# Kernel tuning notes

Hardware: AMD Instinct MI355X
Metric: run time of the kernel (lower is better)

The kernel has to match this reference:

```python
import jax, jax.numpy as jnp
import numpy as np

S, T, B = 120, 10, 128          # sentence len, word len, batch
E, HW, HS = 80, 75, 700         # embedding, word-GRU hidden, sentence-GRU hidden
V = 30000                       # vocab size


def gru_scan(x, Wih, Whh, bih, bhh):
    """Single-direction GRU (PyTorch gate math). x: [T, N, in] -> (ys [T,N,H], h_T [N,H])."""
    H = Whh.shape[-1]
    xw = jnp.einsum('tni,gi->tng', x, Wih) + bih  # precompute input gates [T,N,3H]

    def step(h, xw_t):
        gh = h @ Whh.T + bhh
        r = jax.nn.sigmoid(xw_t[..., :H] + gh[..., :H])
        z = jax.nn.sigmoid(xw_t[..., H:2 * H] + gh[..., H:2 * H])
        n = jnp.tanh(xw_t[..., 2 * H:] + r * gh[..., 2 * H:])
        h_new = (1.0 - z) * n + z * h
        return h_new, h_new

    h0 = jnp.zeros((x.shape[1], H), x.dtype)
    hT, ys = jax.lax.scan(step, h0, xw)
    return ys, hT


def bigru_layer(x, Wih, Whh, bih, bhh):
    """Bidirectional GRU layer; params have leading dir axis [2,...]."""
    yf, hf = gru_scan(x, Wih[0], Whh[0], bih[0], bhh[0])
    yb, hb = gru_scan(x[::-1], Wih[1], Whh[1], bih[1], bhh[1])
    y = jnp.concatenate([yf, yb[::-1]], axis=-1)
    return y, hf, hb


def setup_inputs() -> dict:
    key = jax.random.key(0)
    ks = iter(jax.random.split(key, 40))

    def p(shape):
        return jax.random.normal(next(ks), shape, jnp.float32) * 0.05

    inp = {'x': jax.random.randint(next(ks), (S, T, B), 0, V)}
    inp['emb'] = p((V, E))
    # word encoder: 2-layer bi-GRU, layer0 in=E, layer1 in=2*HW
    inp['we_Wih0'] = p((2, 3 * HW, E)); inp['we_Whh0'] = p((2, 3 * HW, HW))
    inp['we_bih0'] = p((2, 3 * HW)); inp['we_bhh0'] = p((2, 3 * HW))
    inp['we_Wih1'] = p((2, 3 * HW, 2 * HW)); inp['we_Whh1'] = p((2, 3 * HW, HW))
    inp['we_bih1'] = p((2, 3 * HW)); inp['we_bhh1'] = p((2, 3 * HW))
    # sentence encoder: 2-layer bi-GRU, layer0 in=4*HW=300, layer1 in=2*HS
    inp['se_Wih0'] = p((2, 3 * HS, 4 * HW)); inp['se_Whh0'] = p((2, 3 * HS, HS))
    inp['se_bih0'] = p((2, 3 * HS)); inp['se_bhh0'] = p((2, 3 * HS))
    inp['se_Wih1'] = p((2, 3 * HS, 2 * HS)); inp['se_Whh1'] = p((2, 3 * HS, HS))
    inp['se_bih1'] = p((2, 3 * HS)); inp['se_bhh1'] = p((2, 3 * HS))
    return inp


def reference(x, emb,
              we_Wih0, we_Whh0, we_bih0, we_bhh0,
              we_Wih1, we_Whh1, we_bih1, we_bhh1,
              se_Wih0, se_Whh0, se_bih0, se_bhh0,
              se_Wih1, se_Whh1, se_bih1, se_bhh1):
    # Fold the python loop over 120 sentence positions into the batch:
    # x [S,T,B] -> [T, S*B]
    xt = jnp.transpose(x, (1, 0, 2)).reshape(T, S * B)
    xe = emb[xt]  # [T, S*B, E]
    y0, hf0, hb0 = bigru_layer(xe, we_Wih0, we_Whh0, we_bih0, we_bhh0)
    _, hf1, hb1 = bigru_layer(y0, we_Wih1, we_Whh1, we_bih1, we_bhh1)
    # torch h stacking: [l0_fwd, l0_bwd, l1_fwd, l1_bwd] concat on feature dim
    words = jnp.concatenate([hf0, hb0, hf1, hb1], axis=-1)  # [S*B, 4*HW]
    words = words.reshape(S, B, 4 * HW)
    y0s, sf0, sb0 = bigru_layer(words, se_Wih0, se_Whh0, se_bih0, se_bhh0)
    _, sf1, sb1 = bigru_layer(y0s, se_Wih1, se_Whh1, se_bih1, se_bhh1)
    h = jnp.concatenate([sf0, sb0, sf1, sb1], axis=-1)[None]  # [1, B, 4*HS]
    return h
```

## Files before the change

### kernel.cpp

```cpp
#include <hip/hip_runtime.h>
#include <hip/hip_bf16.h>

typedef __hip_bfloat16 bf16;
typedef __attribute__((ext_vector_type(8))) short bf16x8;
typedef __attribute__((ext_vector_type(4))) short bf16x4;
typedef __attribute__((ext_vector_type(4))) float f32x4;

__device__ __forceinline__ void stC(float* p, float v) { *p = v; }
__device__ __forceinline__ void stC(bf16* p, float v)  { *p = __float2bfloat16(v); }

__device__ __forceinline__ short f2s(float f) {
    bf16 b = __float2bfloat16(f);
    return __builtin_bit_cast(short, b);
}

__device__ __forceinline__ float sigm(float x) {
    x = fminf(fmaxf(x, -40.f), 40.f);
    return 1.f / (1.f + expf(-x));
}
__device__ __forceinline__ float tanh_s(float x) {
    x = fminf(fmaxf(x, -20.f), 20.f);
    float e = expf(2.f * x);
    return 1.f - 2.f / (e + 1.f);
}

__device__ __forceinline__ bf16x8 ld8(const bf16* p) {
    return *reinterpret_cast<const bf16x8*>(p);
}
__device__ __forceinline__ bf16x8 ld8(const float* p) {
    const float4 f0 = *reinterpret_cast<const float4*>(p);
    const float4 f1 = *reinterpret_cast<const float4*>(p + 4);
    bf16x8 v;
    v[0] = f2s(f0.x); v[1] = f2s(f0.y); v[2] = f2s(f0.z); v[3] = f2s(f0.w);
    v[4] = f2s(f1.x); v[5] = f2s(f1.y); v[6] = f2s(f1.z); v[7] = f2s(f1.w);
    return v;
}
__device__ __forceinline__ bf16x8 ld8_8B(const bf16* p) {
    bf16x4 lo = *reinterpret_cast<const bf16x4*>(p);
    bf16x4 hi = *reinterpret_cast<const bf16x4*>(p + 4);
    bf16x8 v;
    v[0] = lo[0]; v[1] = lo[1]; v[2] = lo[2]; v[3] = lo[3];
    v[4] = hi[0]; v[5] = hi[1]; v[6] = hi[2]; v[7] = hi[3];
    return v;
}

__global__ void f2b(const float* __restrict__ src, bf16* __restrict__ dst, long n) {
    long i = (long)blockIdx.x * 256 + threadIdx.x;
    if (i < n) dst[i] = __float2bfloat16(src[i]);
}
__global__ void f2bpad(const float* __restrict__ src, bf16* __restrict__ dst,
                       int rows, int Ks, int Kd) {
    long i = (long)blockIdx.x * 256 + threadIdx.x;
    if (i >= (long)rows * Kd) return;
    int c = i % Kd; long r = i / Kd;
    dst[i] = __float2bfloat16(c < Ks ? src[r * Ks + c] : 0.f);
}
__global__ void f2bremap(const float* __restrict__ src, bf16* __restrict__ dst, int rows) {
    long i = (long)blockIdx.x * 256 + threadIdx.x;
    if (i >= (long)rows * 160) return;
    int c = i % 160; long r = i / 160;
    float v = 0.f;
    if (c < 75) v = src[r * 150 + c];
    else if (c >= 80 && c < 155) v = src[r * 150 + c - 5];
    dst[i] = __float2bfloat16(v);
}

#define MBM 128
#define MBN 64
#define MLD 40

__global__ __launch_bounds__(256) void gemm_mfma(
    const float* __restrict__ A, long sAd,
    const float* __restrict__ W, long sWd,
    bf16* __restrict__ C, long sCd,
    int M, int Nc, int K)
{
    __shared__ bf16 As[MBM * MLD];
    __shared__ bf16 Ws[MBN * MLD];
    const int d = blockIdx.z;
    A += (long)d * sAd; W += (long)d * sWd; C += (long)d * sCd;
    const int m0 = blockIdx.y * MBM;
    const int n0 = blockIdx.x * MBN;
    const int tid = threadIdx.x;
    const int w = tid >> 6, l = tid & 63;
    const int lr = l & 15, lq = l >> 4;

    f32x4 acc[2][4] = {};
    for (int k0 = 0; k0 < K; k0 += 32) {
#pragma unroll
        for (int i = 0; i < 2; ++i) {
            int u = tid + i * 256;
            int r = u >> 2, kk = (u & 3) * 8;
            bf16x8 v = {};
            if (m0 + r < M && k0 + kk < K)
                v = ld8(A + (long)(m0 + r) * K + k0 + kk);
            *reinterpret_cast<bf16x8*>(&As[r * MLD + kk]) = v;
        }
        {
            int r = tid >> 2, kk = (tid & 3) * 8;
            bf16x8 v = {};
            if (n0 + r < Nc && k0 + kk < K)
                v = ld8(W + (long)(n0 + r) * K + k0 + kk);
            *reinterpret_cast<bf16x8*>(&Ws[r * MLD + kk]) = v;
        }
        __syncthreads();
        bf16x8 af[2], bw[4];
        af[0] = *reinterpret_cast<const bf16x8*>(&As[(w * 32 + lr) * MLD + lq * 8]);
        af[1] = *reinterpret_cast<const bf16x8*>(&As[(w * 32 + 16 + lr) * MLD + lq * 8]);
#pragma unroll
        for (int ni = 0; ni < 4; ++ni)
            bw[ni] = *reinterpret_cast<const bf16x8*>(&Ws[(ni * 16 + lr) * MLD + lq * 8]);
#pragma unroll
        for (int mi = 0; mi < 2; ++mi)
#pragma unroll
            for (int ni = 0; ni < 4; ++ni)
                acc[mi][ni] = __builtin_amdgcn_mfma_f32_16x16x32_bf16(
                    af[mi], bw[ni], acc[mi][ni], 0, 0, 0);
        __syncthreads();
    }
#pragma unroll
    for (int mi = 0; mi < 2; ++mi)
#pragma unroll
        for (int reg = 0; reg < 4; ++reg) {
            int m = m0 + w * 32 + mi * 16 + lq * 4 + reg;
            if (m >= M) continue;
#pragma unroll
            for (int ni = 0; ni < 4; ++ni) {
                int n = n0 + ni * 16 + lr;
                if (n < Nc) stC(&C[(long)m * Nc + n], acc[mi][ni][reg]);
            }
        }
}

__global__ __launch_bounds__(256) void gemm_bt(
    const bf16* __restrict__ A, long sAd,
    const bf16* __restrict__ W, long sWd,
    bf16* __restrict__ C, long sCd,
    int M, int Nc, int KP)
{
    __shared__ bf16 As[128 * 64];
    __shared__ bf16 Ws[128 * 64];
    const int d = blockIdx.z;
    A += (long)d * sAd; W += (long)d * sWd; C += (long)d * sCd;
    const int nx = (Nc + 127) >> 7, ny = M >> 7;
    int id = blockIdx.x;
    int band = id / (8 * ny);
    int rr = id - band * 8 * ny;
    int bwd = nx - band * 8; if (bwd > 8) bwd = 8;
    const int bx = band * 8 + rr % bwd;
    const int by = rr / bwd;
    const int m0 = by << 7;
    const int n0 = bx << 7;
    const int tid = threadIdx.x;
    const int w = tid >> 6, l = tid & 63;
    const int lr = l & 15, lq = l >> 4;

    const int sr = tid >> 3;
    const int sg = tid & 7;
    const bf16x8 z8 = {};
    bf16x8 ra[4], rb[4];
    auto stage = [&](int k0) {
        const bool kin = (k0 + sg * 8) < KP;
#pragma unroll
        for (int i = 0; i < 4; ++i)
            ra[i] = kin ? ld8(A + (long)(m0 + sr + i * 32) * KP + k0 + sg * 8) : z8;
#pragma unroll
        for (int i = 0; i < 4; ++i)
            rb[i] = kin ? ld8(W + (long)(n0 + sr + i * 32) * KP + k0 + sg * 8) : z8;
    };

    f32x4 acc[2][8] = {};
    stage(0);
    for (int k0 = 0; k0 < KP; k0 += 64) {
#pragma unroll
        for (int i = 0; i < 4; ++i) {
            const int r = sr + i * 32;
            const int g = sg ^ (r & 7);
            *reinterpret_cast<bf16x8*>(&As[r * 64 + g * 8]) = ra[i];
            *reinterpret_cast<bf16x8*>(&Ws[r * 64 + g * 8]) = rb[i];
        }
        __syncthreads();
        if (k0 + 64 < KP) stage(k0 + 64);
#pragma unroll
        for (int ks = 0; ks < 2; ++ks) {
            const int gb = ks * 4 + lq;
            bf16x8 af[2], bw8[8];
#pragma unroll
            for (int mi = 0; mi < 2; ++mi) {
                const int r = w * 32 + mi * 16 + lr;
                af[mi] = *reinterpret_cast<const bf16x8*>(
                    &As[r * 64 + (gb ^ (r & 7)) * 8]);
            }
#pragma unroll
            for (int ni = 0; ni < 8; ++ni) {
                const int r = ni * 16 + lr;
                bw8[ni] = *reinterpret_cast<const bf16x8*>(
                    &Ws[r * 64 + (gb ^ (r & 7)) * 8]);
            }
#pragma unroll
            for (int mi = 0; mi < 2; ++mi)
#pragma unroll
                for (int ni = 0; ni < 8; ++ni)
                    acc[mi][ni] = __builtin_amdgcn_mfma_f32_16x16x32_bf16(
                        af[mi], bw8[ni], acc[mi][ni], 0, 0, 0);
        }
        __syncthreads();
    }
#pragma unroll
    for (int mi = 0; mi < 2; ++mi)
#pragma unroll
        for (int reg = 0; reg < 4; ++reg) {
            int m = m0 + w * 32 + mi * 16 + lq * 4 + reg;
#pragma unroll
            for (int ni = 0; ni < 8; ++ni) {
                int n = n0 + ni * 16 + lr;
                if (n < Nc) C[(long)m * Nc + n] = __float2bfloat16(acc[mi][ni][reg]);
            }
        }
}

#define NKS 22
#define HBPE (2 * 128 * 700)

struct StepJob {
    const bf16* Whh;
    const bf16* xw;
    const float* bih;
    const float* bhh;
    float* h;
    const bf16* hr;
    bf16* hw;
    bf16* y;
    int te0, te1;
    int tl0, tl1;
};

__global__ __launch_bounds__(512) void gru_step_sent2(StepJob ja, StepJob jb, int Cbuf)
{
    extern __shared__ bf16 Wlds[];
    const StepJob J = blockIdx.y ? jb : ja;
    const int jt = blockIdx.x, d = blockIdx.z;
    const int tid = threadIdx.x;
    const int w = tid >> 6, l = tid & 63;
    const int lr = l & 15, lq = l >> 4;
    const int j0c = jt * 16;
    const int jcol = j0c + lr;
    const bool jok = jcol < 700;

    const bf16* Wd = J.Whh + (long)d * 2100 * 700;
    bf16x8 wreg[9];
#pragma unroll
    for (int i = 0; i < 9; ++i) {
        int u = tid + i * 512;
        if (u < NKS * 3 * 64) {
            int lane = u & 63;
            int g = (u >> 6) % 3;
            int kk = u / (3 * 64);
            int row = j0c + (lane & 15);
            int k = kk * 32 + (lane >> 4) * 8;
            bf16x8 v = {};
            if (row < 700) {
                const bf16* p = Wd + (long)(g * 700 + row) * 700 + k;
                if (k + 8 <= 700) {
                    v = ld8_8B(p);
                } else {
#pragma unroll
                    for (int t = 0; t < 8; ++t)
                        if (k + t < 700) v[t] = __builtin_bit_cast(short, p[t]);
                }
            }
            wreg[i] = v;
        }
    }

    const int arow = w * 16 + lr;
    const bf16* Ab = J.hr + ((long)d * 128 + arow) * 700;
    bf16x8 areg[NKS];
#pragma unroll
    for (int kk = 0; kk < NKS; ++kk) {
        const int kb = kk * 32 + lq * 8;
        if (kb + 8 <= 700) {
            areg[kk] = ld8_8B(Ab + kb);
        } else {
            bf16x8 v = {};
            bf16x4 lo = *reinterpret_cast<const bf16x4*>(Ab + kb);
            v[0] = lo[0]; v[1] = lo[1]; v[2] = lo[2]; v[3] = lo[3];
            areg[kk] = v;
        }
    }

    const int te = d ? J.te1 : J.te0;
    const int tl = d ? J.tl1 : J.tl0;
    const bf16* xbase = J.xw + ((long)d * Cbuf + tl) * 128 * 2100;
    bf16 xg[3][4];
#pragma unroll
    for (int reg = 0; reg < 4; ++reg) {
        const int m = w * 16 + lq * 4 + reg;
        const bf16* xp = xbase + (long)m * 2100 + jcol;
#pragma unroll
        for (int g = 0; g < 3; ++g) xg[g][reg] = jok ? xp[g * 700] : bf16(0.f);
    }
    const int jc = jok ? jcol : 699;
    const float bir = J.bih[d * 2100 + jc];
    const float biz = J.bih[d * 2100 + 700 + jc];
    const float bin = J.bih[d * 2100 + 1400 + jc];
    const float bhr = J.bhh[d * 2100 + jc];
    const float bhz = J.bhh[d * 2100 + 700 + jc];
    const float bhn = J.bhh[d * 2100 + 1400 + jc];

#pragma unroll
    for (int i = 0; i < 9; ++i) {
        int u = tid + i * 512;
        if (u < NKS * 3 * 64)
            *reinterpret_cast<bf16x8*>(&Wlds[u * 8]) = wreg[i];
    }
    __syncthreads();

    f32x4 acc[3] = {};
#pragma unroll
    for (int kk = 0; kk < NKS; ++kk)
#pragma unroll
        for (int g = 0; g < 3; ++g) {
            bf16x8 b = *reinterpret_cast<const bf16x8*>(&Wlds[((kk * 3 + g) * 64 + l) * 8]);
            acc[g] = __builtin_amdgcn_mfma_f32_16x16x32_bf16(areg[kk], b, acc[g], 0, 0, 0);
        }

    if (jok) {
#pragma unroll
        for (int reg = 0; reg < 4; ++reg) {
            const int m = w * 16 + lq * 4 + reg;
            float r  = sigm((float)xg[0][reg] + bir + acc[0][reg] + bhr);
            float z  = sigm((float)xg[1][reg] + biz + acc[1][reg] + bhz);
            float nn = tanh_s((float)xg[2][reg] + bin + r * (acc[2][reg] + bhn));
            const long hidx = ((long)d * 128 + m) * 700 + jcol;
            const float hnew = (1.f - z) * nn + z * J.h[hidx];
            J.h[hidx] = hnew;
            J.hw[hidx] = __float2bfloat16(hnew);
            if (J.y) J.y[((long)te * 128 + m) * 1408 + (long)d * 700 + jcol] =
                         __float2bfloat16(hnew);
        }
    }
}

#define WNW 15360

__global__ __launch_bounds__(512) void gru_word0_fused(
    const int* __restrict__ x,
    const bf16* __restrict__ embW,
    const bf16* __restrict__ Whh,
    const float* __restrict__ bih,
    const float* __restrict__ bhh,
    const bf16* __restrict__ hr,
    bf16* __restrict__ hw,
    float* __restrict__ h,
    bf16* __restrict__ y,
    int T, int k)
{
    __shared__ bf16 Wl[3 * 3 * 64 * 8];
    const int jt = blockIdx.x, mt = blockIdx.y, d = blockIdx.z;
    const int tid = threadIdx.x;
    const int w = tid >> 6, l = tid & 63;
    const int lr = l & 15, lq = l >> 4;
    const int j0c = jt * 16, jcol = j0c + lr;
    const bool jok = jcol < 75;
    const int t_eff = d ? (T - 1 - k) : k;

    const int na = mt * 128 + w * 16 + lr;
    const bf16* Ab = hr + ((long)d * WNW + na) * 96;
    bf16x8 areg[3];
#pragma unroll
    for (int kk = 0; kk < 3; ++kk) areg[kk] = ld8(Ab + kk * 32 + lq * 8);

    float xg[3][4];
#pragma unroll
    for (int reg = 0; reg < 4; ++reg) {
        const int m = mt * 128 + w * 16 + lq * 4 + reg;
        const int s = m >> 7, b = m & 127;
        int tok = x[(s * T + t_eff) * 128 + b];
        tok = max(0, min(29999, tok));
        const bf16* ep = embW + ((long)d * 30000 + tok) * 225;
#pragma unroll
        for (int g = 0; g < 3; ++g)
            xg[g][reg] = jok ? (float)ep[g * 75 + jcol] : 0.f;
    }
    const int jc = jok ? jcol : 74;
    const float bir = bih[d*225+jc], biz = bih[d*225+75+jc], bin = bih[d*225+150+jc];
    const float bhr = bhh[d*225+jc], bhz = bhh[d*225+75+jc], bhn = bhh[d*225+150+jc];

    const bf16* Wd = Whh + (long)d * 225 * 80;
    for (int u = tid; u < 3 * 3 * 64; u += 512) {
        int lane = u & 63;
        int g = (u >> 6) % 3;
        int kk = u / 192;
        int row = j0c + (lane & 15);
        int kb = kk * 32 + (lane >> 4) * 8;
        bf16x8 v = {};
        if (row < 75 && kb < 80) v = ld8_8B(Wd + (long)(g * 75 + row) * 80 + kb);
        *reinterpret_cast<bf16x8*>(&Wl[u * 8]) = v;
    }
    __syncthreads();

    f32x4 acc[3] = {};
#pragma unroll
    for (int kk = 0; kk < 3; ++kk)
#pragma unroll
        for (int g = 0; g < 3; ++g) {
            bf16x8 b8 = *reinterpret_cast<const bf16x8*>(&Wl[((kk*3+g)*64 + l)*8]);
            acc[g] = __builtin_amdgcn_mfma_f32_16x16x32_bf16(areg[kk], b8, acc[g], 0, 0, 0);
        }

    if (jok) {
#pragma unroll
        for (int reg = 0; reg < 4; ++reg) {
            const int m = mt * 128 + w * 16 + lq * 4 + reg;
            float r  = sigm(xg[0][reg] + bir + acc[0][reg] + bhr);
            float z  = sigm(xg[1][reg] + biz + acc[1][reg] + bhz);
            float nn = tanh_s(xg[2][reg] + bin + r * (acc[2][reg] + bhn));
            const long hif = ((long)d * WNW + m) * 75 + jcol;
            const float hnew = (1.f - z) * nn + z * h[hif];
            h[hif] = hnew;
            hw[((long)d * WNW + m) * 96 + jcol] = __float2bfloat16(hnew);
            y[((long)t_eff * WNW + m) * 160 + d * 80 + jcol] = __float2bfloat16(hnew);
        }
    }
}

__global__ __launch_bounds__(512) void gru_word1_fused(
    const bf16* __restrict__ y0,
    const bf16* __restrict__ Wih,
    const bf16* __restrict__ Whh,
    const float* __restrict__ bih,
    const float* __restrict__ bhh,
    const bf16* __restrict__ hr,
    bf16* __restrict__ hw,
    float* __restrict__ h,
    int T, int k)
{
    __shared__ bf16 Wl[8 * 3 * 64 * 8];
    const int jt = blockIdx.x, mt = blockIdx.y, d = blockIdx.z;
    const int tid = threadIdx.x;
    const int w = tid >> 6, l = tid & 63;
    const int lr = l & 15, lq = l >> 4;
    const int j0c = jt * 16, jcol = j0c + lr;
    const bool jok = jcol < 75;
    const int t_eff = d ? (T - 1 - k) : k;

    const int na = mt * 128 + w * 16 + lr;
    const bf16* A1 = y0 + ((long)t_eff * WNW + na) * 160;
    bf16x8 a1[5];
#pragma unroll
    for (int kk = 0; kk < 5; ++kk) a1[kk] = ld8(A1 + kk * 32 + lq * 8);
    const bf16* A2 = hr + ((long)d * WNW + na) * 96;
    bf16x8 a2[3];
#pragma unroll
    for (int kk = 0; kk < 3; ++kk) a2[kk] = ld8(A2 + kk * 32 + lq * 8);

    const int jc = jok ? jcol : 74;
    const float bir = bih[d*225+jc], biz = bih[d*225+75+jc], bin = bih[d*225+150+jc];
    const float bhr = bhh[d*225+jc], bhz = bhh[d*225+75+jc], bhn = bhh[d*225+150+jc];

    const bf16* Wx = Wih + (long)d * 225 * 160;
    for (int u = tid; u < 960; u += 512) {
        int lane = u & 63;
        int g = (u >> 6) % 3;
        int kk = u / 192;
        int row = j0c + (lane & 15);
        int kb = kk * 32 + (lane >> 4) * 8;
        bf16x8 v = {};
        if (row < 75) v = ld8(Wx + (long)(g * 75 + row) * 160 + kb);
        *reinterpret_cast<bf16x8*>(&Wl[u * 8]) = v;
    }
    const bf16* Wd = Whh + (long)d * 225 * 80;
    for (int u = tid; u < 576; u += 512) {
        int lane = u & 63;
        int g = (u >> 6) % 3;
        int kk = u / 192;
        int row = j0c + (lane & 15);
        int kb = kk * 32 + (lane >> 4) * 8;
        bf16x8 v = {};
        if (row < 75 && kb < 80) v = ld8_8B(Wd + (long)(g * 75 + row) * 80 + kb);
        *reinterpret_cast<bf16x8*>(&Wl[(960 + u) * 8]) = v;
    }
    __syncthreads();

    f32x4 ax[3] = {}, ah[3] = {};
#pragma unroll
    for (int kk = 0; kk < 5; ++kk)
#pragma unroll
        for (int g = 0; g < 3; ++g) {
            bf16x8 b8 = *reinterpret_cast<const bf16x8*>(&Wl[((kk*3+g)*64 + l)*8]);
            ax[g] = __builtin_amdgcn_mfma_f32_16x16x32_bf16(a1[kk], b8, ax[g], 0, 0, 0);
        }
#pragma unroll
    for (int kk = 0; kk < 3; ++kk)
#pragma unroll
        for (int g = 0; g < 3; ++g) {
            bf16x8 b8 = *reinterpret_cast<const bf16x8*>(&Wl[(960 + (kk*3+g)*64 + l)*8]);
            ah[g] = __builtin_amdgcn_mfma_f32_16x16x32_bf16(a2[kk], b8, ah[g], 0, 0, 0);
        }

    if (jok) {
#pragma unroll
        for (int reg = 0; reg < 4; ++reg) {
            const int m = mt * 128 + w * 16 + lq * 4 + reg;
            float r  = sigm(ax[0][reg] + bir + ah[0][reg] + bhr);
            float z  = sigm(ax[1][reg] + biz + ah[1][reg] + bhz);
            float nn = tanh_s(ax[2][reg] + bin + r * (ah[2][reg] + bhn));
            const long hif = ((long)d * WNW + m) * 75 + jcol;
            const float hnew = (1.f - z) * nn + z * h[hif];
            h[hif] = hnew;
            hw[((long)d * WNW + m) * 96 + jcol] = __float2bfloat16(hnew);
        }
    }
}

template <typename OT>
__global__ void concat4(const float* __restrict__ ha, const float* __restrict__ hb,
                        OT* __restrict__ out, int N, int H, int OS)
{
    long idx = (long)blockIdx.x * 256 + threadIdx.x;
    int C4 = 4 * H;
    if (idx >= (long)N * C4) return;
    int c = idx % C4;
    long n = idx / C4;
    int blk = c / H, j = c % H;
    const float* src = (blk < 2) ? ha : hb;
    int dd = blk & 1;
    stC(&out[n * (long)OS + c], src[((long)dd * N + n) * H + j]);
}

extern "C" void kernel_launch(void* const* d_in, const int* in_sizes, int n_in,
                              void* d_out, int out_size, void* d_ws, size_t ws_size,
                              hipStream_t stream)
{
    const int S = 120, T = 10, B = 128, E = 80, HW = 75, HS = 700, V = 30000;
    const int Nw = S * B;
    const int Gw = 3 * HW;
    const int Gs = 3 * HS;
    (void)in_sizes; (void)n_in; (void)out_size; (void)ws_size;

    const int*   x       = (const int*)d_in[0];
    const float* emb     = (const float*)d_in[1];
    const float* we_Wih0 = (const float*)d_in[2],  *we_Whh0 = (const float*)d_in[3];
    const float* we_bih0 = (const float*)d_in[4],  *we_bhh0 = (const float*)d_in[5];
    const float* we_Wih1 = (const float*)d_in[6],  *we_Whh1 = (const float*)d_in[7];
    const float* we_bih1 = (const float*)d_in[8],  *we_bhh1 = (const float*)d_in[9];
    const float* se_Wih0 = (const float*)d_in[10], *se_Whh0 = (const float*)d_in[11];
    const float* se_bih0 = (const float*)d_in[12], *se_bhh0 = (const float*)d_in[13];
    const float* se_Wih1 = (const float*)d_in[14], *se_Whh1 = (const float*)d_in[15];
    const float* se_bih1 = (const float*)d_in[16], *se_bhh1 = (const float*)d_in[17];

    char* ws = (char*)d_ws;
    const size_t oP1 = 9340000;
    const size_t oP2 = oP1 + 49152000;
    const size_t oP3 = oP2 + 43008000;
    const size_t total = oP3 + 30516480;

    bf16*  words  = (bf16*)ws;
    bf16*  y0w    = (bf16*)(ws + oP1);
    bf16*  embW   = (bf16*)(ws + oP2);
    float* h_w0   = (float*)(ws + oP3);
    float* h_w1   = (float*)(ws + oP3 + 9216000);
    bf16*  pingW  = (bf16*)(ws + oP3 + 18432000);
    bf16*  Whh0bw = (bf16*)(ws + oP3 + 30228480);
    bf16*  Whh1bw = (bf16*)(ws + oP3 + 30300480);
    bf16*  Wih1pw = (bf16*)(ws + oP3 + 30372480);
    const long PWE = 2L * Nw * 96;
    bf16*  y0s    = (bf16*)(ws + oP1);
    bf16*  bufL0  = (bf16*)(ws + oP2);
    bf16*  bufL1  = (bf16*)(ws + oP2 + 21504000);
    bf16*  Whh0b  = (bf16*)(ws + oP3);
    bf16*  Whh1b  = (bf16*)(ws + oP3 + 5880000);
    bf16*  hbf0   = (bf16*)(ws + oP3 + 11760000);
    bf16*  hbf1   = (bf16*)(ws + oP3 + 12476800);
    float* h_s0   = (float*)(ws + oP3 + 13193600);
    float* h_s1   = (float*)(ws + oP3 + 13910400);
    bf16*  Wih0p  = (bf16*)(ws + oP3 + 14627200);
    bf16*  Wih1p  = (bf16*)(ws + oP3 + 17273216);

    hipMemsetAsync(ws, 0, oP2, stream);
    hipMemsetAsync(ws + oP3, 0, 30516480, stream);

    gemm_mfma<<<dim3((Gw + MBN - 1) / MBN, (V + MBM - 1) / MBM, 2), 256, 0, stream>>>(
        emb, 0, we_Wih0, (long)Gw * E, embW, (long)V * Gw, V, Gw, E);
    for (int d = 0; d < 2; ++d) {
        f2bpad<<<(225 * 80 + 255) / 256, 256, 0, stream>>>(
            we_Whh0 + (long)d * 225 * 75, Whh0bw + (long)d * 225 * 80, 225, 75, 80);
        f2bpad<<<(225 * 80 + 255) / 256, 256, 0, stream>>>(
            we_Whh1 + (long)d * 225 * 75, Whh1bw + (long)d * 225 * 80, 225, 75, 80);
        f2bremap<<<(225 * 160 + 255) / 256, 256, 0, stream>>>(
            we_Wih1 + (long)d * 225 * 150, Wih1pw + (long)d * 225 * 160, 225);
    }
    dim3 wgrid(5, Nw / 128, 2);
    for (int k = 0; k < T; ++k) {
        int p = k & 1;
        gru_word0_fused<<<wgrid, 512, 0, stream>>>(
            x, embW, Whh0bw, we_bih0, we_bhh0,
            pingW + (long)p * PWE, pingW + (long)(p ^ 1) * PWE, h_w0, y0w, T, k);
    }
    hipMemsetAsync(pingW, 0, 11796480, stream);
    for (int k = 0; k < T; ++k) {
        int p = k & 1;
        gru_word1_fused<<<wgrid, 512, 0, stream>>>(
            y0w, Wih1pw, Whh1bw, we_bih1, we_bhh1,
            pingW + (long)p * PWE, pingW + (long)(p ^ 1) * PWE, h_w1, T, k);
    }
    {
        long tot = (long)Nw * 4 * HW;
        concat4<bf16><<<(tot + 255) / 256, 256, 0, stream>>>(h_w0, h_w1, words, Nw, HW, 304);
    }

    {
        long nwh = 2LL * Gs * HS;
        f2b<<<(nwh + 255) / 256, 256, 0, stream>>>(se_Whh0, Whh0b, nwh);
        f2b<<<(nwh + 255) / 256, 256, 0, stream>>>(se_Whh1, Whh1b, nwh);
        for (int d = 0; d < 2; ++d) {
            f2bpad<<<((long)2100 * 304 + 255) / 256, 256, 0, stream>>>(
                se_Wih0 + (long)d * 2100 * 300, Wih0p + (long)d * 2176 * 304, 2100, 300, 304);
            f2bpad<<<((long)2100 * 1408 + 255) / 256, 256, 0, stream>>>(
                se_Wih1 + (long)d * 2100 * 1400, Wih1p + (long)d * 2176 * 1408, 2100, 1400, 1408);
        }
    }
    hipMemsetAsync(ws + oP3 + 11760000, 0, 2867200, stream);

    const unsigned ldsBytes = (unsigned)(NKS * 3 * 64 * 8 * sizeof(bf16));
    const int C2 = 20, NC = 6;
    const int nblk = ((Gs + 127) / 128) * ((C2 * B) / 128);

    for (int t = 0; t <= NC; ++t) {
        if (t < NC) {
            int tb0 = t * C2, tb1 = S - t * C2 - C2;
            gemm_bt<<<dim3(nblk, 1, 2), 256, 0, stream>>>(
                words + (long)tb0 * B * 304, (long)(tb1 - tb0) * B * 304,
                Wih0p, (long)2176 * 304,
                bufL0, (long)C2 * B * Gs, C2 * B, Gs, 304);
        }
        if (t >= 1) {
            int c = t - 1, tb0 = c * C2, tb1 = S - c * C2 - C2;
            gemm_bt<<<dim3(nblk, 1, 2), 256, 0, stream>>>(
                y0s + (long)tb0 * B * 1408, (long)(tb1 - tb0) * B * 1408,
                Wih1p, (long)2176 * 1408,
                bufL1, (long)C2 * B * Gs, C2 * B, Gs, 1408);
        }
        for (int i = 0; i < C2; ++i) {
            StepJob jobs[2]; int nj = 0;
            if (t < NC) {
                int k = t * C2 + i;
                StepJob J;
                J.Whh = Whh0b; J.xw = bufL0; J.bih = se_bih0; J.bhh = se_bhh0;
                J.h = h_s0;
                int p = k & 1;
                J.hr = hbf0 + (long)p * HBPE; J.hw = hbf0 + (long)(p ^ 1) * HBPE;
                J.y = y0s;
                J.te0 = k; J.te1 = S - 1 - k; J.tl0 = i; J.tl1 = C2 - 1 - i;
                jobs[nj++] = J;
            }
            if (t >= 1) {
                int k = (t - 1) * C2 + i;
                StepJob J;
                J.Whh = Whh1b; J.xw = bufL1; J.bih = se_bih1; J.bhh = se_bhh1;
                J.h = h_s1;
                int p = k & 1;
                J.hr = hbf1 + (long)p * HBPE; J.hw = hbf1 + (long)(p ^ 1) * HBPE;
                J.y = nullptr;
                J.te0 = k; J.te1 = S - 1 - k; J.tl0 = i; J.tl1 = C2 - 1 - i;
                jobs[nj++] = J;
            }
            if (nj == 1) jobs[1] = jobs[0];
            gru_step_sent2<<<dim3(44, nj, 2), 512, ldsBytes, stream>>>(
                jobs[0], jobs[1], C2);
        }
    }

    {
        long tot = (long)B * 4 * HS;
        concat4<float><<<(tot + 255) / 256, 256, 0, stream>>>(
            h_s0, h_s1, (float*)d_out, B, HS, 4 * HS);
    }
}
```

Before: 3.224 ms.

## Load GEMM and recurrent-weight tiles straight into LDS with global_load_lds

```diff
diff --git a/kernel.cpp b/kernel.cpp
--- a/kernel.cpp
+++ b/kernel.cpp
@@ -12,6 +12,12 @@
 __device__ __forceinline__ short f2s(float f) {
     bf16 b = __float2bfloat16(f);
     return __builtin_bit_cast(short, b);
+}
+
+__device__ __forceinline__ void gload16(const void* gp, void* lp) {
+    __builtin_amdgcn_global_load_lds(
+        (const __attribute__((address_space(1))) void*)gp,
+        (__attribute__((address_space(3))) void*)lp, 16, 0, 0);
 }
 
 __device__ __forceinline__ float sigm(float x) {
@@ -155,32 +161,26 @@
     const int w = tid >> 6, l = tid & 63;
     const int lr = l & 15, lq = l >> 4;
 
-    const int sr = tid >> 3;
-    const int sg = tid & 7;
-    const bf16x8 z8 = {};
-    bf16x8 ra[4], rb[4];
-    auto stage = [&](int k0) {
-        const bool kin = (k0 + sg * 8) < KP;
-#pragma unroll
-        for (int i = 0; i < 4; ++i)
-            ra[i] = kin ? ld8(A + (long)(m0 + sr + i * 32) * KP + k0 + sg * 8) : z8;
-#pragma unroll
-        for (int i = 0; i < 4; ++i)
-            rb[i] = kin ? ld8(W + (long)(n0 + sr + i * 32) * KP + k0 + sg * 8) : z8;
-    };
+    int rof[4], cof[4];
+#pragma unroll
+    for (int j = 0; j < 4; ++j) {
+        int G = (w * 4 + j) * 64 + l;
+        int r = G >> 3, g = G & 7;
+        rof[j] = r;
+        cof[j] = (g ^ (r & 7)) * 8;
+    }
 
     f32x4 acc[2][8] = {};
-    stage(0);
     for (int k0 = 0; k0 < KP; k0 += 64) {
 #pragma unroll
-        for (int i = 0; i < 4; ++i) {
-            const int r = sr + i * 32;
-            const int g = sg ^ (r & 7);
-            *reinterpret_cast<bf16x8*>(&As[r * 64 + g * 8]) = ra[i];
-            *reinterpret_cast<bf16x8*>(&Ws[r * 64 + g * 8]) = rb[i];
-        }
+        for (int j = 0; j < 4; ++j)
+            gload16(A + (long)(m0 + rof[j]) * KP + k0 + cof[j],
+                    &As[(w * 4 + j) * 512]);
+#pragma unroll
+        for (int j = 0; j < 4; ++j)
+            gload16(W + (long)(n0 + rof[j]) * KP + k0 + cof[j],
+                    &Ws[(w * 4 + j) * 512]);
         __syncthreads();
-        if (k0 + 64 < KP) stage(k0 + 64);
 #pragma unroll
         for (int ks = 0; ks < 2; ++ks) {
             const int gb = ks * 4 + lq;
@@ -231,6 +231,7 @@
     const bf16* hr;
     bf16* hw;
     bf16* y;
+    const bf16* zb;
     int te0, te1;
     int tl0, tl1;
 };
@@ -248,28 +249,20 @@
     const bool jok = jcol < 700;
 
     const bf16* Wd = J.Whh + (long)d * 2100 * 700;
-    bf16x8 wreg[9];
-#pragma unroll
-    for (int i = 0; i < 9; ++i) {
-        int u = tid + i * 512;
-        if (u < NKS * 3 * 64) {
-            int lane = u & 63;
-            int g = (u >> 6) % 3;
-            int kk = u / (3 * 64);
-            int row = j0c + (lane & 15);
-            int k = kk * 32 + (lane >> 4) * 8;
-            bf16x8 v = {};
-            if (row < 700) {
-                const bf16* p = Wd + (long)(g * 700 + row) * 700 + k;
-                if (k + 8 <= 700) {
-                    v = ld8_8B(p);
-                } else {
-#pragma unroll
-                    for (int t = 0; t < 8; ++t)
-                        if (k + t < 700) v[t] = __builtin_bit_cast(short, p[t]);
-                }
+    {
+        const int row = j0c + lr;
+        const int kof = lq * 8;
+#pragma unroll
+        for (int i = 0; i < 9; ++i) {
+            const int issue = w + i * 8;
+            if (issue < 66) {
+                const int g = issue % 3;
+                const int kk = issue / 3;
+                const bf16* src = (row < 700)
+                    ? Wd + (long)(g * 700 + row) * 700 + kk * 32 + kof
+                    : J.zb;
+                gload16(src, &Wlds[(long)issue * 512]);
             }
-            wreg[i] = v;
         }
     }
 
@@ -308,12 +301,6 @@
     const float bhz = J.bhh[d * 2100 + 700 + jc];
     const float bhn = J.bhh[d * 2100 + 1400 + jc];
 
-#pragma unroll
-    for (int i = 0; i < 9; ++i) {
-        int u = tid + i * 512;
-        if (u < NKS * 3 * 64)
-            *reinterpret_cast<bf16x8*>(&Wlds[u * 8]) = wreg[i];
-    }
     __syncthreads();
 
     f32x4 acc[3] = {};
@@ -551,10 +538,11 @@
     const float* se_bih1 = (const float*)d_in[16], *se_bhh1 = (const float*)d_in[17];
 
     char* ws = (char*)d_ws;
-    const size_t oP1 = 9340000;
+    const size_t oP1 = 9830400;
     const size_t oP2 = oP1 + 49152000;
     const size_t oP3 = oP2 + 43008000;
-    const size_t total = oP3 + 30516480;
+    const size_t r4  = 30516480;
+    const size_t total = oP3 + r4 + 256;
 
     bf16*  words  = (bf16*)ws;
     bf16*  y0w    = (bf16*)(ws + oP1);
@@ -576,10 +564,11 @@
     float* h_s0   = (float*)(ws + oP3 + 13193600);
     float* h_s1   = (float*)(ws + oP3 + 13910400);
     bf16*  Wih0p  = (bf16*)(ws + oP3 + 14627200);
-    bf16*  Wih1p  = (bf16*)(ws + oP3 + 17273216);
+    bf16*  Wih1p  = (bf16*)(ws + oP3 + 17412480);
+    const bf16* zscr = (const bf16*)(ws + oP3 + r4);
 
     hipMemsetAsync(ws, 0, oP2, stream);
-    hipMemsetAsync(ws + oP3, 0, 30516480, stream);
+    hipMemsetAsync(ws + oP3, 0, r4 + 256, stream);
 
     gemm_mfma<<<dim3((Gw + MBN - 1) / MBN, (V + MBM - 1) / MBM, 2), 256, 0, stream>>>(
         emb, 0, we_Wih0, (long)Gw * E, embW, (long)V * Gw, V, Gw, E);
@@ -607,7 +596,7 @@
     }
     {
         long tot = (long)Nw * 4 * HW;
-        concat4<bf16><<<(tot + 255) / 256, 256, 0, stream>>>(h_w0, h_w1, words, Nw, HW, 304);
+        concat4<bf16><<<(tot + 255) / 256, 256, 0, stream>>>(h_w0, h_w1, words, Nw, HW, 320);
     }
 
     {
@@ -615,15 +604,15 @@
         f2b<<<(nwh + 255) / 256, 256, 0, stream>>>(se_Whh0, Whh0b, nwh);
         f2b<<<(nwh + 255) / 256, 256, 0, stream>>>(se_Whh1, Whh1b, nwh);
         for (int d = 0; d < 2; ++d) {
-            f2bpad<<<((long)2100 * 304 + 255) / 256, 256, 0, stream>>>(
-                se_Wih0 + (long)d * 2100 * 300, Wih0p + (long)d * 2176 * 304, 2100, 300, 304);
+            f2bpad<<<((long)2100 * 320 + 255) / 256, 256, 0, stream>>>(
+                se_Wih0 + (long)d * 2100 * 300, Wih0p + (long)d * 2176 * 320, 2100, 300, 320);
             f2bpad<<<((long)2100 * 1408 + 255) / 256, 256, 0, stream>>>(
                 se_Wih1 + (long)d * 2100 * 1400, Wih1p + (long)d * 2176 * 1408, 2100, 1400, 1408);
         }
     }
     hipMemsetAsync(ws + oP3 + 11760000, 0, 2867200, stream);
 
-    const unsigned ldsBytes = (unsigned)(NKS * 3 * 64 * 8 * sizeof(bf16));
+    const unsigned ldsBytes = 67584;
     const int C2 = 20, NC = 6;
     const int nblk = ((Gs + 127) / 128) * ((C2 * B) / 128);
 
@@ -631,9 +620,9 @@
         if (t < NC) {
             int tb0 = t * C2, tb1 = S - t * C2 - C2;
             gemm_bt<<<dim3(nblk, 1, 2), 256, 0, stream>>>(
-                words + (long)tb0 * B * 304, (long)(tb1 - tb0) * B * 304,
-                Wih0p, (long)2176 * 304,
-                bufL0, (long)C2 * B * Gs, C2 * B, Gs, 304);
+                words + (long)tb0 * B * 320, (long)(tb1 - tb0) * B * 320,
+                Wih0p, (long)2176 * 320,
+                bufL0, (long)C2 * B * Gs, C2 * B, Gs, 320);
         }
         if (t >= 1) {
             int c = t - 1, tb0 = c * C2, tb1 = S - c * C2 - C2;
@@ -651,7 +640,7 @@
                 J.h = h_s0;
                 int p = k & 1;
                 J.hr = hbf0 + (long)p * HBPE; J.hw = hbf0 + (long)(p ^ 1) * HBPE;
-                J.y = y0s;
+                J.y = y0s; J.zb = zscr;
                 J.te0 = k; J.te1 = S - 1 - k; J.tl0 = i; J.tl1 = C2 - 1 - i;
                 jobs[nj++] = J;
             }
@@ -662,7 +651,7 @@
                 J.h = h_s1;
                 int p = k & 1;
                 J.hr = hbf1 + (long)p * HBPE; J.hw = hbf1 + (long)(p ^ 1) * HBPE;
-                J.y = nullptr;
+                J.y = nullptr; J.zb = zscr;
                 J.te0 = k; J.te1 = S - 1 - k; J.tl0 = i; J.tl1 = C2 - 1 - i;
                 jobs[nj++] = J;
             }
```

New measurement: 3.251 ms. About the same (+0.8%).
